# Kernel tuning notes

Measured on AMD Instinct MI355X. Metric: run time of the kernel, lower is better.

## Reference

```python
import jax, jax.numpy as jnp
import numpy as np

TOP_K = 5
EPS = 1e-12  # F.normalize eps

def _l2_normalize(v):
    n = jnp.linalg.norm(v, axis=-1, keepdims=True)
    return v / jnp.maximum(n, EPS)

def setup_inputs() -> dict:
    key = jax.random.key(0)
    k1, k2 = jax.random.split(key)
    B, S, C, M = 4, 2048, 512, 32768
    x = jax.random.normal(k1, (B, S, C), dtype=jnp.float32)
    # xavier_uniform-ish init for the memory table
    bound = np.sqrt(6.0 / (M + C)).astype(np.float32)
    memory_mean = jax.random.uniform(k2, (M, C), dtype=jnp.float32, minval=-bound, maxval=bound)
    return {"x": x, "memory_mean": memory_mean}

def reference(x, memory_mean):
    B, S, C = x.shape
    Mmat = memory_mean  # deterministic=True -> _sample_M returns memory_mean
    q = x.reshape(-1, C)                      # [BS, C]
    qn = _l2_normalize(q)
    mn = _l2_normalize(Mmat)                  # [M, C]
    sim = qn @ mn.T                           # [BS, M] cosine similarity
    scores, idx = jax.lax.top_k(sim, TOP_K)   # [BS, K]
    w = jax.nn.softmax(scores, axis=-1)       # [BS, K]
    gathered = Mmat[idx]                      # [BS, K, C]
    retrieved = jnp.einsum('bk,bkc->bc', w, gathered).reshape(B, S, C)
    out = x + 0.5 * retrieved
    return out
```

## Files before the change

kernel.cpp:

```cpp
#include <hip/hip_runtime.h>
#include <hip/hip_bf16.h>
#include <math.h>

using f32x4 = __attribute__((ext_vector_type(4))) float;
typedef unsigned char u8;

#define BS    8192
#define CDIM  512
#define MROWS 32768
#define NC    8
#define CHUNK (MROWS / NC)
#define TN    32
#define TQ    128
#define KTOP  5
#define ITERS (CHUNK / TN)
#define ROWB  512
#define KEY_INIT 0x3FFF8000u

__device__ __forceinline__ unsigned enc_key(float s, int n) {
    unsigned u = __float_as_uint(s);
    u ^= (unsigned)((int)u >> 31) | 0x80000000u;
    return (u & 0xFFFF8000u) | (unsigned)n;
}
__device__ __forceinline__ float dec_score(unsigned k) {
    unsigned u = k & 0xFFFF8000u;
    u = (u & 0x80000000u) ? (u ^ 0x80000000u) : ~u;
    return __uint_as_float(u);
}

__device__ __forceinline__ void ins_nb(unsigned (&ks)[KTOP], unsigned k) {
    unsigned t = k;
#pragma unroll
    for (int j = 0; j < KTOP; ++j) {
        unsigned hi = t > ks[j] ? t : ks[j];
        unsigned lo = t > ks[j] ? ks[j] : t;
        ks[j] = hi; t = lo;
    }
}

__device__ __forceinline__ float dpp_fmax16(float x) {
    int t;
    t = __builtin_amdgcn_update_dpp(0, __float_as_int(x), 0xB1, 0xF, 0xF, true);
    x = fmaxf(x, __int_as_float(t));
    t = __builtin_amdgcn_update_dpp(0, __float_as_int(x), 0x4E, 0xF, 0xF, true);
    x = fmaxf(x, __int_as_float(t));
    t = __builtin_amdgcn_update_dpp(0, __float_as_int(x), 0x141, 0xF, 0xF, true);
    x = fmaxf(x, __int_as_float(t));
    t = __builtin_amdgcn_update_dpp(0, __float_as_int(x), 0x140, 0xF, 0xF, true);
    x = fmaxf(x, __int_as_float(t));
    return x;
}

__global__ void nrm_cast2(const float* __restrict__ memM, u8* __restrict__ mn,
                          const float* __restrict__ x, u8* __restrict__ qn) {
    int wave = threadIdx.x >> 6, lane = threadIdx.x & 63;
    int row = blockIdx.x * 4 + wave;
    const float* in;
    u8* out;
    if (row < MROWS) { in = memM + (size_t)row * CDIM; out = mn + (size_t)row * ROWB; }
    else             { int r = row - MROWS; in = x + (size_t)r * CDIM; out = qn + (size_t)r * ROWB; }
    const float* rp = in + lane * 8;
    float4 v0 = *(const float4*)rp;
    float4 v1 = *(const float4*)(rp + 4);
    float ss = v0.x * v0.x + v0.y * v0.y + v0.z * v0.z + v0.w * v0.w
             + v1.x * v1.x + v1.y * v1.y + v1.z * v1.z + v1.w * v1.w;
#pragma unroll
    for (int d = 1; d < 64; d <<= 1) ss += __shfl_xor(ss, d);
    float sc = 1.0f / fmaxf(sqrtf(ss), 1e-12f);
    int lo = __builtin_amdgcn_cvt_pk_fp8_f32(v0.x * sc, v0.y * sc, 0, false);
    lo     = __builtin_amdgcn_cvt_pk_fp8_f32(v0.z * sc, v0.w * sc, lo, true);
    int hi = __builtin_amdgcn_cvt_pk_fp8_f32(v1.x * sc, v1.y * sc, 0, false);
    hi     = __builtin_amdgcn_cvt_pk_fp8_f32(v1.z * sc, v1.w * sc, hi, true);
    uint2 o; o.x = (unsigned)lo; o.y = (unsigned)hi;
    *(uint2*)(out + lane * 8) = o;
}

__device__ __forceinline__ void stage_tile(const u8* __restrict__ mn, int nb,
                                           u8* buf, int wave, int lane) {
    const int r0 = wave * 8;
    const int li = lane & 31, half = lane >> 5;
#pragma unroll
    for (int j = 0; j < 4; ++j) {
        const int row = r0 + 2 * j + half;
        const u8* src = mn + (size_t)(nb + row) * ROWB + ((li ^ (row & 7)) * 16);
        __builtin_amdgcn_global_load_lds(
            (const __attribute__((address_space(1))) void*)src,
            (__attribute__((address_space(3))) void*)(buf + (r0 + 2 * j) * ROWB),
            16, 0, 0);
    }
}

__global__ __launch_bounds__(256, 2) void simtopk(
        const u8* __restrict__ qn, const u8* __restrict__ mn,
        unsigned* __restrict__ cand) {
    __shared__ __align__(16) u8 Bt[2][TN * ROWB];

    const int tid  = threadIdx.x;
    const int wave = tid >> 6, lane = tid & 63;
    const int quad = lane >> 4, c16 = lane & 15;
    const int nc = blockIdx.x;
    const int qt = blockIdx.y;
    const int qw = qt * TQ + wave * 32;
    const int nb0 = nc * CHUNK;

    long2 a[2][8];
#pragma unroll
    for (int s = 0; s < 2; ++s) {
        const u8* p = qn + (size_t)(qw + s * 16 + c16) * ROWB + quad * 16;
#pragma unroll
        for (int t = 0; t < 8; ++t)
            a[s][t] = *(const long2*)(p + t * 64);
    }

    unsigned keys[8][KTOP];
    float thr[8];
#pragma unroll
    for (int l = 0; l < 8; ++l) {
        thr[l] = -2.0f;
#pragma unroll
        for (int j = 0; j < KTOP; ++j) keys[l][j] = KEY_INIT;
    }

    const int sw = c16 & 7;

    stage_tile(mn, nb0, &Bt[0][0], wave, lane);

    for (int it = 0; it < ITERS; ++it) {
        __syncthreads();
        if (it + 1 < ITERS)
            stage_tile(mn, nb0 + (it + 1) * TN, &Bt[(it + 1) & 1][0], wave, lane);

        const u8* bb = &Bt[it & 1][c16 * ROWB];
        f32x4 acc00 = {0.f, 0.f, 0.f, 0.f}, acc01 = {0.f, 0.f, 0.f, 0.f};
        f32x4 acc10 = {0.f, 0.f, 0.f, 0.f}, acc11 = {0.f, 0.f, 0.f, 0.f};
#pragma unroll
        for (int t = 0; t < 8; ++t) {
            const int slot = ((t * 4 + quad) ^ sw) * 16;
            long2 b0 = *(const long2*)(bb + slot);
            long2 b1 = *(const long2*)(bb + 16 * ROWB + slot);
            acc00 = __builtin_amdgcn_mfma_f32_16x16x32_fp8_fp8(a[0][t].x, b0.x, acc00, 0, 0, 0);
            acc00 = __builtin_amdgcn_mfma_f32_16x16x32_fp8_fp8(a[0][t].y, b0.y, acc00, 0, 0, 0);
            acc01 = __builtin_amdgcn_mfma_f32_16x16x32_fp8_fp8(a[0][t].x, b1.x, acc01, 0, 0, 0);
            acc01 = __builtin_amdgcn_mfma_f32_16x16x32_fp8_fp8(a[0][t].y, b1.y, acc01, 0, 0, 0);
            acc10 = __builtin_amdgcn_mfma_f32_16x16x32_fp8_fp8(a[1][t].x, b0.x, acc10, 0, 0, 0);
            acc10 = __builtin_amdgcn_mfma_f32_16x16x32_fp8_fp8(a[1][t].y, b0.y, acc10, 0, 0, 0);
            acc11 = __builtin_amdgcn_mfma_f32_16x16x32_fp8_fp8(a[1][t].x, b1.x, acc11, 0, 0, 0);
            acc11 = __builtin_amdgcn_mfma_f32_16x16x32_fp8_fp8(a[1][t].y, b1.y, acc11, 0, 0, 0);
        }

        const int nb = nb0 + it * TN;
        const int n0 = nb + c16, n1 = nb + 16 + c16;
#pragma unroll
        for (int j = 0; j < 4; ++j) {
            if (acc00[j] > thr[j])     ins_nb(keys[j],     enc_key(acc00[j], n0));
            if (acc01[j] > thr[j])     ins_nb(keys[j],     enc_key(acc01[j], n1));
            if (acc10[j] > thr[4 + j]) ins_nb(keys[4 + j], enc_key(acc10[j], n0));
            if (acc11[j] > thr[4 + j]) ins_nb(keys[4 + j], enc_key(acc11[j], n1));
        }
        if ((it & 3) == 3) {
#pragma unroll
            for (int l = 0; l < 8; ++l)
                thr[l] = dpp_fmax16(fmaxf(thr[l], dec_score(keys[l][KTOP - 1])));
        }
    }

#pragma unroll
    for (int d = 1; d <= 8; d <<= 1) {
#pragma unroll
        for (int l = 0; l < 8; ++l) {
            unsigned rk[KTOP];
#pragma unroll
            for (int j = 0; j < KTOP; ++j) rk[j] = (unsigned)__shfl_xor((int)keys[l][j], d);
#pragma unroll
            for (int j = 0; j < KTOP; ++j) ins_nb(keys[l], rk[j]);
        }
    }

#pragma unroll
    for (int l = 0; l < 8; ++l) {
        if (c16 == l) {
            const int q = qw + (l >> 2) * 16 + quad * 4 + (l & 3);
            unsigned* cp = cand + ((size_t)q * NC + nc) * KTOP;
#pragma unroll
            for (int j = 0; j < KTOP; ++j) cp[j] = keys[l][j];
        }
    }
}

__global__ void epilogue(const float* __restrict__ x, const float* __restrict__ mem,
                         const unsigned* __restrict__ cand, float* __restrict__ out) {
    int wave = threadIdx.x >> 6, lane = threadIdx.x & 63;
    int q = blockIdx.x * 4 + wave;

    unsigned key = (lane < NC * KTOP) ? cand[(size_t)q * (NC * KTOP) + lane] : 0u;
    float s[KTOP]; int id[KTOP];
#pragma unroll
    for (int k = 0; k < KTOP; ++k) {
        unsigned m = key;
#pragma unroll
        for (int d = 32; d; d >>= 1) {
            unsigned o = (unsigned)__shfl_xor((int)m, d);
            m = o > m ? o : m;
        }
        s[k] = dec_score(m);
        id[k] = (int)(m & 0x7FFFu);
        unsigned long long b = __ballot(key == m);
        int first = __ffsll((long long)b) - 1;
        if (lane == first) key = 0u;
    }
    float w[KTOP], sum = 0.f;
#pragma unroll
    for (int k = 0; k < KTOP; ++k) { w[k] = expf(s[k] - s[0]); sum += w[k]; }
    float inv = 0.5f / sum;

    int c = lane * 8;
    const float4* xp = (const float4*)(x + (size_t)q * CDIM + c);
    float4 o0 = xp[0], o1 = xp[1];
#pragma unroll
    for (int k = 0; k < KTOP; ++k) {
        float wk = w[k] * inv;
        const float4* mp = (const float4*)(mem + (size_t)id[k] * CDIM + c);
        float4 g0 = mp[0], g1 = mp[1];
        o0.x += wk * g0.x; o0.y += wk * g0.y; o0.z += wk * g0.z; o0.w += wk * g0.w;
        o1.x += wk * g1.x; o1.y += wk * g1.y; o1.z += wk * g1.z; o1.w += wk * g1.w;
    }
    float* op = out + (size_t)q * CDIM + c;
    *(float4*)op = o0;
    *(float4*)(op + 4) = o1;
}

extern "C" void kernel_launch(void* const* d_in, const int* in_sizes, int n_in,
                              void* d_out, int out_size, void* d_ws, size_t ws_size,
                              hipStream_t stream) {
    const float* x    = (const float*)d_in[0];
    const float* memM = (const float*)d_in[1];
    float* out = (float*)d_out;

    u8* mn = (u8*)d_ws;
    u8* qn = mn + (size_t)MROWS * ROWB;
    unsigned* cand = (unsigned*)(qn + (size_t)BS * ROWB);

    nrm_cast2<<<(MROWS + BS) / 4, 256, 0, stream>>>(memM, mn, x, qn);
    simtopk<<<dim3(NC, BS / TQ), 256, 0, stream>>>(qn, mn, cand);
    epilogue<<<BS / 4, 256, 0, stream>>>(x, memM, cand, out);
}
```

Measured before the change: 372.2 us.

## Use scaled 16x16x128 FP8 MFMA and double memory tile width

Replaces the 16x16x32 FP8 MFMA chain with the gfx950 scaled 16x16x128 f8f6f4 MFMA using unit scales, which cuts the instruction count per tile by four. The memory tile grows from 32 to 64 rows per iteration, so each stage moves twice the LDS data and there are half as many barriers. Query fragments and LDS reads are re-laid out as 32-byte chunks to match the new operand shape. The threshold refresh interval is rescaled to keep it roughly constant in memory rows, at the cost of larger LDS use and more accumulator registers per wave, which may reduce occupancy.

```diff
diff --git a/kernel.cpp b/kernel.cpp
--- a/kernel.cpp
+++ b/kernel.cpp
@@ -1,8 +1,9 @@
 #include <hip/hip_runtime.h>
-#include <hip/hip_bf16.h>
 #include <math.h>
 
 using f32x4 = __attribute__((ext_vector_type(4))) float;
+typedef __attribute__((ext_vector_type(4))) int i32x4;
+typedef __attribute__((ext_vector_type(8))) int i32x8;
 typedef unsigned char u8;
 
 #define BS    8192
@@ -10,12 +11,13 @@
 #define MROWS 32768
 #define NC    8
 #define CHUNK (MROWS / NC)
-#define TN    32
+#define TN    64
 #define TQ    128
 #define KTOP  5
 #define ITERS (CHUNK / TN)
 #define ROWB  512
 #define KEY_INIT 0x3FFF8000u
+#define SCL   0x7F7F7F7F
 
 __device__ __forceinline__ unsigned enc_key(float s, int n) {
     unsigned u = __float_as_uint(s);
@@ -77,10 +79,10 @@
 
 __device__ __forceinline__ void stage_tile(const u8* __restrict__ mn, int nb,
                                            u8* buf, int wave, int lane) {
-    const int r0 = wave * 8;
+    const int r0 = wave * 16;
     const int li = lane & 31, half = lane >> 5;
 #pragma unroll
-    for (int j = 0; j < 4; ++j) {
+    for (int j = 0; j < 8; ++j) {
         const int row = r0 + 2 * j + half;
         const u8* src = mn + (size_t)(nb + row) * ROWB + ((li ^ (row & 7)) * 16);
         __builtin_amdgcn_global_load_lds(
@@ -103,13 +105,16 @@
     const int qw = qt * TQ + wave * 32;
     const int nb0 = nc * CHUNK;
 
-    long2 a[2][8];
+    i32x8 a[2][4];
 #pragma unroll
     for (int s = 0; s < 2; ++s) {
-        const u8* p = qn + (size_t)(qw + s * 16 + c16) * ROWB + quad * 16;
-#pragma unroll
-        for (int t = 0; t < 8; ++t)
-            a[s][t] = *(const long2*)(p + t * 64);
+        const u8* p = qn + (size_t)(qw + s * 16 + c16) * ROWB + quad * 32;
+#pragma unroll
+        for (int t = 0; t < 4; ++t) {
+            i32x4 lo = *(const i32x4*)(p + t * 128);
+            i32x4 hi = *(const i32x4*)(p + t * 128 + 16);
+            a[s][t] = __builtin_shufflevector(lo, hi, 0, 1, 2, 3, 4, 5, 6, 7);
+        }
     }
 
     unsigned keys[8][KTOP];
@@ -121,7 +126,9 @@
         for (int j = 0; j < KTOP; ++j) keys[l][j] = KEY_INIT;
     }
 
-    const int sw = c16 & 7;
+    const int sw  = c16 & 7;
+    const int pb0 = c16 * ROWB + (((2 * quad) ^ sw) * 16);
+    const int pb1 = pb0 ^ 16;
 
     stage_tile(mn, nb0, &Bt[0][0], wave, lane);
 
@@ -130,34 +137,38 @@
         if (it + 1 < ITERS)
             stage_tile(mn, nb0 + (it + 1) * TN, &Bt[(it + 1) & 1][0], wave, lane);
 
-        const u8* bb = &Bt[it & 1][c16 * ROWB];
-        f32x4 acc00 = {0.f, 0.f, 0.f, 0.f}, acc01 = {0.f, 0.f, 0.f, 0.f};
-        f32x4 acc10 = {0.f, 0.f, 0.f, 0.f}, acc11 = {0.f, 0.f, 0.f, 0.f};
-#pragma unroll
-        for (int t = 0; t < 8; ++t) {
-            const int slot = ((t * 4 + quad) ^ sw) * 16;
-            long2 b0 = *(const long2*)(bb + slot);
-            long2 b1 = *(const long2*)(bb + 16 * ROWB + slot);
-            acc00 = __builtin_amdgcn_mfma_f32_16x16x32_fp8_fp8(a[0][t].x, b0.x, acc00, 0, 0, 0);
-            acc00 = __builtin_amdgcn_mfma_f32_16x16x32_fp8_fp8(a[0][t].y, b0.y, acc00, 0, 0, 0);
-            acc01 = __builtin_amdgcn_mfma_f32_16x16x32_fp8_fp8(a[0][t].x, b1.x, acc01, 0, 0, 0);
-            acc01 = __builtin_amdgcn_mfma_f32_16x16x32_fp8_fp8(a[0][t].y, b1.y, acc01, 0, 0, 0);
-            acc10 = __builtin_amdgcn_mfma_f32_16x16x32_fp8_fp8(a[1][t].x, b0.x, acc10, 0, 0, 0);
-            acc10 = __builtin_amdgcn_mfma_f32_16x16x32_fp8_fp8(a[1][t].y, b0.y, acc10, 0, 0, 0);
-            acc11 = __builtin_amdgcn_mfma_f32_16x16x32_fp8_fp8(a[1][t].x, b1.x, acc11, 0, 0, 0);
-            acc11 = __builtin_amdgcn_mfma_f32_16x16x32_fp8_fp8(a[1][t].y, b1.y, acc11, 0, 0, 0);
+        const u8* bb = &Bt[it & 1][0];
+        f32x4 acc[2][4];
+#pragma unroll
+        for (int s = 0; s < 2; ++s)
+#pragma unroll
+            for (int h = 0; h < 4; ++h) acc[s][h] = (f32x4){0.f, 0.f, 0.f, 0.f};
+
+#pragma unroll
+        for (int h = 0; h < 4; ++h) {
+#pragma unroll
+            for (int t = 0; t < 4; ++t) {
+                i32x4 lo = *(const i32x4*)(bb + pb0 + h * 8192 + t * 128);
+                i32x4 hi = *(const i32x4*)(bb + pb1 + h * 8192 + t * 128);
+                i32x8 b = __builtin_shufflevector(lo, hi, 0, 1, 2, 3, 4, 5, 6, 7);
+                acc[0][h] = __builtin_amdgcn_mfma_scale_f32_16x16x128_f8f6f4(
+                                a[0][t], b, acc[0][h], 0, 0, 0, SCL, 0, SCL);
+                acc[1][h] = __builtin_amdgcn_mfma_scale_f32_16x16x128_f8f6f4(
+                                a[1][t], b, acc[1][h], 0, 0, 0, SCL, 0, SCL);
+            }
         }
 
         const int nb = nb0 + it * TN;
-        const int n0 = nb + c16, n1 = nb + 16 + c16;
-#pragma unroll
-        for (int j = 0; j < 4; ++j) {
-            if (acc00[j] > thr[j])     ins_nb(keys[j],     enc_key(acc00[j], n0));
-            if (acc01[j] > thr[j])     ins_nb(keys[j],     enc_key(acc01[j], n1));
-            if (acc10[j] > thr[4 + j]) ins_nb(keys[4 + j], enc_key(acc10[j], n0));
-            if (acc11[j] > thr[4 + j]) ins_nb(keys[4 + j], enc_key(acc11[j], n1));
-        }
-        if ((it & 3) == 3) {
+#pragma unroll
+        for (int h = 0; h < 4; ++h) {
+            const int n = nb + 16 * h + c16;
+#pragma unroll
+            for (int j = 0; j < 4; ++j) {
+                if (acc[0][h][j] > thr[j])     ins_nb(keys[j],     enc_key(acc[0][h][j], n));
+                if (acc[1][h][j] > thr[4 + j]) ins_nb(keys[4 + j], enc_key(acc[1][h][j], n));
+            }
+        }
+        if (it & 1) {
 #pragma unroll
             for (int l = 0; l < 8; ++l)
                 thr[l] = dpp_fmax16(fmaxf(thr[l], dec_score(keys[l][KTOP - 1])));
```

Measured after the change: 413.7 us. +11.1%, slower.
